# Kernel optimization log

Hardware: AMD Instinct MI355X
Metric: run time of the kernel (lower is better)

Reference implementation:

```python
import jax, jax.numpy as jnp
import numpy as np

B, D = 16384, 4096

def setup_inputs() -> dict:
    key = jax.random.key(0)
    k1, k2 = jax.random.split(key)
    x1 = jax.random.normal(k1, (B, D), dtype=jnp.float32)
    x2 = jax.random.normal(k2, (B, D), dtype=jnp.float32)
    return {"x1": x1, "x2": x2}

def reference(x1, x2):
    # Faithful to Dis(loss_type='cos').cosine_similarity: the original loops
    # over columns accumulating dot product and squared sums; fused here as
    # single per-row reductions. Accumulators start at zero, so:
    dot = jnp.sum(x1 * x2, axis=1)            # [B]
    sx = jnp.sum(x1 * x1, axis=1)             # [B]
    sy = jnp.sum(x2 * x2, axis=1)             # [B]
    cos = dot / (jnp.sqrt(sx) * jnp.sqrt(sy))
    return 0.5 * cos
```

## Files before the change

kernel.cpp:

```cpp
#include <hip/hip_runtime.h>
#include <hip/hip_bf16.h>

#define B_ROWS 16384
#define D_COLS 4096
#define BLOCK 256

__global__ __launch_bounds__(BLOCK) void cos_sim_kernel(
    const float* __restrict__ x1,
    const float* __restrict__ x2,
    float* __restrict__ out)
{
    const int row = blockIdx.x;
    const size_t base = (size_t)row * D_COLS;
    const float4* __restrict__ r1 = reinterpret_cast<const float4*>(x1 + base);
    const float4* __restrict__ r2 = reinterpret_cast<const float4*>(x2 + base);

    float dot = 0.0f, sx = 0.0f, sy = 0.0f;

#pragma unroll
    for (int it = 0; it < (D_COLS / 4) / BLOCK; ++it) {
        const int j = threadIdx.x + it * BLOCK;
        float4 a = r1[j];
        float4 b = r2[j];
        dot += a.x * b.x + a.y * b.y + a.z * b.z + a.w * b.w;
        sx  += a.x * a.x + a.y * a.y + a.z * a.z + a.w * a.w;
        sy  += b.x * b.x + b.y * b.y + b.z * b.z + b.w * b.w;
    }

#pragma unroll
    for (int off = 32; off > 0; off >>= 1) {
        dot += __shfl_down(dot, off, 64);
        sx  += __shfl_down(sx,  off, 64);
        sy  += __shfl_down(sy,  off, 64);
    }

    __shared__ float sred[3][BLOCK / 64];
    const int wave = threadIdx.x >> 6;
    const int lane = threadIdx.x & 63;
    if (lane == 0) {
        sred[0][wave] = dot;
        sred[1][wave] = sx;
        sred[2][wave] = sy;
    }
    __syncthreads();

    if (threadIdx.x == 0) {
        float d = 0.0f, a = 0.0f, b = 0.0f;
#pragma unroll
        for (int w = 0; w < BLOCK / 64; ++w) {
            d += sred[0][w];
            a += sred[1][w];
            b += sred[2][w];
        }
        out[row] = 0.5f * d / (sqrtf(a) * sqrtf(b));
    }
}

extern "C" void kernel_launch(void* const* d_in, const int* in_sizes, int n_in,
                              void* d_out, int out_size, void* d_ws, size_t ws_size,
                              hipStream_t stream) {
    const float* x1 = (const float*)d_in[0];
    const float* x2 = (const float*)d_in[1];
    float* out = (float*)d_out;

    cos_sim_kernel<<<B_ROWS, BLOCK, 0, stream>>>(x1, x2, out);
}
```

Baseline: 496.0 us.

## Map one wavefront per row and use nontemporal vector loads

Each 64-lane wavefront now reduces a whole row, so the block no longer needs shared memory or a block-wide barrier, and the grid shrinks by four. Loads switch to nontemporal builtins so the streamed inputs are not kept in cache. Each lane now issues 16 float4 loads per input instead of 4, which gives more memory parallelism per wave. This may lower occupancy-driven latency hiding if register use grows.

```diff
diff --git a/kernel.cpp b/kernel.cpp
--- a/kernel.cpp
+++ b/kernel.cpp
@@ -4,24 +4,30 @@
 #define B_ROWS 16384
 #define D_COLS 4096
 #define BLOCK 256
+#define WAVES_PER_BLOCK (BLOCK / 64)
+#define F4_PER_LANE (D_COLS / 4 / 64)
+
+typedef float f32x4 __attribute__((ext_vector_type(4)));
 
 __global__ __launch_bounds__(BLOCK) void cos_sim_kernel(
     const float* __restrict__ x1,
     const float* __restrict__ x2,
     float* __restrict__ out)
 {
-    const int row = blockIdx.x;
+    const int wave = threadIdx.x >> 6;
+    const int lane = threadIdx.x & 63;
+    const int row  = blockIdx.x * WAVES_PER_BLOCK + wave;
     const size_t base = (size_t)row * D_COLS;
-    const float4* __restrict__ r1 = reinterpret_cast<const float4*>(x1 + base);
-    const float4* __restrict__ r2 = reinterpret_cast<const float4*>(x2 + base);
+
+    const f32x4* __restrict__ r1 = reinterpret_cast<const f32x4*>(x1 + base);
+    const f32x4* __restrict__ r2 = reinterpret_cast<const f32x4*>(x2 + base);
 
     float dot = 0.0f, sx = 0.0f, sy = 0.0f;
 
 #pragma unroll
-    for (int it = 0; it < (D_COLS / 4) / BLOCK; ++it) {
-        const int j = threadIdx.x + it * BLOCK;
-        float4 a = r1[j];
-        float4 b = r2[j];
+    for (int it = 0; it < F4_PER_LANE; ++it) {
+        f32x4 a = __builtin_nontemporal_load(&r1[lane + it * 64]);
+        f32x4 b = __builtin_nontemporal_load(&r2[lane + it * 64]);
         dot += a.x * b.x + a.y * b.y + a.z * b.z + a.w * b.w;
         sx  += a.x * a.x + a.y * a.y + a.z * a.z + a.w * a.w;
         sy  += b.x * b.x + b.y * b.y + b.z * b.z + b.w * b.w;
@@ -34,25 +40,8 @@
         sy  += __shfl_down(sy,  off, 64);
     }
 
-    __shared__ float sred[3][BLOCK / 64];
-    const int wave = threadIdx.x >> 6;
-    const int lane = threadIdx.x & 63;
     if (lane == 0) {
-        sred[0][wave] = dot;
-        sred[1][wave] = sx;
-        sred[2][wave] = sy;
-    }
-    __syncthreads();
-
-    if (threadIdx.x == 0) {
-        float d = 0.0f, a = 0.0f, b = 0.0f;
-#pragma unroll
-        for (int w = 0; w < BLOCK / 64; ++w) {
-            d += sred[0][w];
-            a += sred[1][w];
-            b += sred[2][w];
-        }
-        out[row] = 0.5f * d / (sqrtf(a) * sqrtf(b));
+        out[row] = 0.5f * dot / (sqrtf(sx) * sqrtf(sy));
     }
 }
 
@@ -63,5 +52,5 @@
     const float* x2 = (const float*)d_in[1];
     float* out = (float*)d_out;
 
-    cos_sim_kernel<<<B_ROWS, BLOCK, 0, stream>>>(x1, x2, out);
+    cos_sim_kernel<<<B_ROWS / WAVES_PER_BLOCK, BLOCK, 0, stream>>>(x1, x2, out);
 }
```

Result: faster. 468.3 us (-5.6%).
